# Performance work log

Measured on AMD Instinct MI355X. Metric: run time of the kernel, lower is better.

Reference implementation:

```python
import jax, jax.numpy as jnp
import numpy as np

B, S, H = 2, 2048, 2048
NH, NKV, HD = 16, 4, 128
ROPE_BASE = 10000.0


def hbit_linear(x, w):
    # BitNet: 8-bit per-token absmax activation quant, ternary (2-bit) weight quant
    s = 127.0 / jnp.clip(jnp.max(jnp.abs(x), axis=-1, keepdims=True), 1e-5, None)
    xq = jnp.clip(jnp.round(x * s), -128, 127) / s
    ws = 1.0 / jnp.clip(jnp.mean(jnp.abs(w)), 1e-5, None)
    wq = jnp.clip(jnp.round(w * ws), -1, 1) / ws
    return xq @ wq.T


def rotate_half(x):
    h = x.shape[-1] // 2
    return jnp.concatenate([-x[..., h:], x[..., :h]], axis=-1)


def rope_cos_sin(position_ids, head_dim, dtype):
    inv_freq = 1.0 / (ROPE_BASE ** (jnp.arange(0, head_dim, 2, dtype=jnp.float32) / head_dim))
    freqs = position_ids.astype(jnp.float32)[..., None] * inv_freq[None, None, :]  # (b,s,hd/2)
    emb = jnp.concatenate([freqs, freqs], axis=-1)  # (b,s,hd)
    return jnp.cos(emb).astype(dtype)[:, :, None, :], jnp.sin(emb).astype(dtype)[:, :, None, :]


def setup_inputs() -> dict:
    key = jax.random.key(0)
    ks = jax.random.split(key, 5)
    xavier = lambda k, shp: jax.random.uniform(k, shp, jnp.float32, -1.0, 1.0) * np.sqrt(6.0 / (shp[0] + shp[1]))
    causal = jnp.where(jnp.tril(jnp.ones((S, S), bool)), 0.0, -1e9).astype(jnp.float32)[None, None]
    return {
        "hidden_states": jax.random.normal(ks[0], (B, S, H), jnp.float32),
        "attention_mask": causal,
        "Wq": xavier(ks[1], (H, H)),
        "Wk": xavier(ks[2], (NKV * HD, H)),
        "Wv": xavier(ks[3], (NKV * HD, H)),
        "Wo": xavier(ks[4], (H, H)),
        "position_ids": jnp.arange(S, dtype=jnp.int64 if jax.config.jax_enable_x64 else jnp.int32)[None, :],
    }


def reference(hidden_states, attention_mask, Wq, Wk, Wv, Wo, position_ids):
    b, s, _ = hidden_states.shape
    q = hbit_linear(hidden_states, Wq).reshape(b, s, NH, HD)
    k = hbit_linear(hidden_states, Wk).reshape(b, s, NKV, HD)
    v = hbit_linear(hidden_states, Wv).reshape(b, s, NKV, HD)
    cos, sin = rope_cos_sin(position_ids, HD, q.dtype)  # (1,s,1,hd)
    q = q * cos + rotate_half(q) * sin
    k = k * cos + rotate_half(k) * sin
    n_rep = NH // NKV
    k = jnp.repeat(k, n_rep, axis=2)  # (b,s,NH,hd)
    v = jnp.repeat(v, n_rep, axis=2)
    scale = 1.0 / np.sqrt(HD)
    scores = jnp.einsum("bqhd,bkhd->bhqk", q, k) * scale + attention_mask
    probs = jax.nn.softmax(scores, axis=-1)  # dropout inactive (eval)
    out = jnp.einsum("bhqk,bkhd->bqhd", probs, v).reshape(b, s, NH * HD)
    return hbit_linear(out, Wo)
```

## Files before the change

### kernel.cpp

```cpp
#include <hip/hip_runtime.h>
#include <hip/hip_bf16.h>

#define B_ 2
#define S_ 2048
#define H_ 2048
#define NH_ 16
#define NKV_ 4
#define HD_ 128
#define M_ (B_*S_)
#define KVD_ (NKV_*HD_)
#define PSTR 40
#define GRID_MEGA 768

typedef signed char s8;
typedef __attribute__((ext_vector_type(8))) short short8;
typedef __attribute__((ext_vector_type(4))) float f32x4;
typedef __attribute__((ext_vector_type(4))) int int4v;

__device__ __forceinline__ float loadf(const void* p, long i, int isb){
  if (isb) return __bfloat162float(((const __hip_bfloat16*)p)[i]);
  return ((const float*)p)[i];
}

__device__ __forceinline__ unsigned short f2bf(float f){
  union { float f; unsigned u; } v; v.f = f;
  unsigned r = v.u + 0x7FFF + ((v.u >> 16) & 1);
  return (unsigned short)(r >> 16);
}

__device__ __forceinline__ float bf2f(unsigned short b){
  union { unsigned u; float f; } v; v.u = ((unsigned)b) << 16; return v.f;
}

__device__ __forceinline__ void gl2lds16(const void* g, void* l){
  __builtin_amdgcn_global_load_lds(
      (const __attribute__((address_space(1))) void*)g,
      (__attribute__((address_space(3))) void*)l, 16, 0, 0);
}

__device__ __forceinline__ void gridbar(unsigned* bar, unsigned target){
  __syncthreads();
  if (threadIdx.x == 0){
    __threadfence();
    atomicAdd(bar, 1u);
    unsigned guard = 0;
    while (atomicAdd(bar, 0u) < target){
      __builtin_amdgcn_s_sleep(2);
      if (++guard > (1u<<22)) break;
    }
    __threadfence();
  }
  __syncthreads();
}

__device__ __forceinline__ int detect_isb_s(const unsigned int* x, int* dsh){
  int t = threadIdx.x, cnt = 0;
  #pragma unroll
  for (int i = 0; i < 8; i++){
    unsigned e = (x[t + i*256] >> 7) & 0xFF;
    cnt += (e >= 90 && e <= 150) ? 1 : 0;
  }
  #pragma unroll
  for (int k = 32; k > 0; k >>= 1) cnt += __shfl_down(cnt, k, 64);
  if ((t & 63) == 0) dsh[t >> 6] = cnt;
  __syncthreads();
  int r = (dsh[0] + dsh[1] + dsh[2] + dsh[3]) > 1228;
  __syncthreads();
  return r;
}

__device__ __forceinline__ void wscan_seg(const void* w, long n, long b0, int nb,
                                          int isb, float* wsum_i, float* sh){
  int t = threadIdx.x;
  float s = 0.f;
  for (long i = b0*256 + t; i < n; i += (long)nb*256) s += fabsf(loadf(w, i, isb));
  sh[t] = s; __syncthreads();
  for (int k = 128; k > 0; k >>= 1){ if (t < k) sh[t] += sh[t+k]; __syncthreads(); }
  if (t == 0) atomicAdd(wsum_i, sh[0]);
  __syncthreads();
}

__device__ __forceinline__ void wquant_seg(const void* w, s8* out, long n, long b0, int nb,
                                           float mean, int isb){
  int t = threadIdx.x;
  float sc = 1.0f / mean;
  for (long i = b0*256 + t; i < n; i += (long)nb*256){
    float v = rintf(loadf(w, i, isb) * sc);
    v = fminf(fmaxf(v, -1.f), 1.f);
    out[i] = (s8)v;
  }
}

__device__ __forceinline__ void aquant_row_x(const void* x, int isb, long r,
                                             float* srow, s8* xq, float* sh){
  int t = threadIdx.x;
  long base = r * H_;
  float v[8];
  if (isb){
    uint4 wv = ((const uint4*)((const unsigned short*)x + base))[t];
    unsigned u[4] = {wv.x, wv.y, wv.z, wv.w};
    #pragma unroll
    for (int i = 0; i < 4; i++){
      v[2*i]   = bf2f((unsigned short)(u[i] & 0xFFFF));
      v[2*i+1] = bf2f((unsigned short)(u[i] >> 16));
    }
  } else {
    const float4* p = (const float4*)((const float*)x + base);
    float4 a = p[t*2], b2 = p[t*2+1];
    v[0]=a.x; v[1]=a.y; v[2]=a.z; v[3]=a.w; v[4]=b2.x; v[5]=b2.y; v[6]=b2.z; v[7]=b2.w;
  }
  float mx = 0.f;
  #pragma unroll
  for (int i = 0; i < 8; i++) mx = fmaxf(mx, fabsf(v[i]));
  sh[t] = mx; __syncthreads();
  for (int k = 128; k > 0; k >>= 1){ if (t < k) sh[t] = fmaxf(sh[t], sh[t+k]); __syncthreads(); }
  float s = 127.0f / fmaxf(sh[0], 1e-5f);
  if (t == 0) srow[r] = s;
  unsigned long long pk = 0;
  #pragma unroll
  for (int i = 0; i < 8; i++){
    float q = fminf(fmaxf(rintf(v[i] * s), -128.f), 127.f);
    pk |= ((unsigned long long)(unsigned char)(s8)q) << (8*i);
  }
  *(unsigned long long*)(xq + base + t*8) = pk;
  __syncthreads();
}

__device__ __forceinline__ void aquant_row_ab(const unsigned short* x, long r,
                                              float* srow, s8* xq, float* sh){
  int t = threadIdx.x;
  long base = r * H_;
  uint4 wv = ((const uint4*)(x + base))[t];
  unsigned u[4] = {wv.x, wv.y, wv.z, wv.w};
  float v[8];
  #pragma unroll
  for (int i = 0; i < 4; i++){
    v[2*i]   = bf2f((unsigned short)(u[i] & 0xFFFF));
    v[2*i+1] = bf2f((unsigned short)(u[i] >> 16));
  }
  float mx = 0.f;
  #pragma unroll
  for (int i = 0; i < 8; i++) mx = fmaxf(mx, fabsf(v[i]));
  sh[t] = mx; __syncthreads();
  for (int k = 128; k > 0; k >>= 1){ if (t < k) sh[t] = fmaxf(sh[t], sh[t+k]); __syncthreads(); }
  float s = 127.0f / fmaxf(sh[0], 1e-5f);
  if (t == 0) srow[r] = s;
  unsigned long long pk = 0;
  #pragma unroll
  for (int i = 0; i < 8; i++){
    float q = fminf(fmaxf(rintf(v[i] * s), -128.f), 127.f);
    pk |= ((unsigned long long)(unsigned char)(s8)q) << (8*i);
  }
  *(unsigned long long*)(xq + base + t*8) = pk;
  __syncthreads();
}

__device__ __forceinline__ void gemm_core(
      const s8* __restrict__ A, const s8* __restrict__ Bw, s8* As, s8* Bs,
      const float* __restrict__ srow, float mean,
      void* __restrict__ Cout, int N, int mode, int isb,
      unsigned short* __restrict__ Vt,
      const float* __restrict__ ct, const float* __restrict__ st,
      long bcol, long arow){
  int tid = threadIdx.x;
  int wave = tid >> 6, lane = tid & 63;
  int quad = lane >> 4, c = lane & 15;
  int wm = wave >> 1, wn = wave & 1;
  const int K = H_;

  int4v acc[4][4];
  #pragma unroll
  for (int mt = 0; mt < 4; mt++)
    #pragma unroll
    for (int nt = 0; nt < 4; nt++) acc[mt][nt] = (int4v){0,0,0,0};

  int rl = lane >> 2;
  int kq = (lane & 3) ^ ((lane >> 3) & 3);
  int ch0 = wave*2, ch1 = wave*2 + 1;
  long gA0 = (arow + ch0*16 + rl)*(long)K + kq*16;
  long gA1 = (arow + ch1*16 + rl)*(long)K + kq*16;
  long gB0 = (bcol + ch0*16 + rl)*(long)K + kq*16;
  long gB1 = (bcol + ch1*16 + rl)*(long)K + kq*16;

  int sA = quad ^ ((c >> 1) & 3);
  int ntl[4];
  #pragma unroll
  for (int nt = 0; nt < 4; nt++) ntl[nt] = 2*wn + (nt & 1) + 4*(nt >> 1);
  int frA[4], frB[4];
  #pragma unroll
  for (int mt = 0; mt < 4; mt++) frA[mt] = (wm*64 + mt*16 + c)*64 + sA*16;
  #pragma unroll
  for (int nt = 0; nt < 4; nt++) frB[nt] = (ntl[nt]*16 + c)*64 + sA*16;

  for (int k0 = 0; k0 < K; k0 += 128){
    gl2lds16(A  + gA0 + k0,      As        + ch0*1024);
    gl2lds16(A  + gA1 + k0,      As        + ch1*1024);
    gl2lds16(Bw + gB0 + k0,      Bs        + ch0*1024);
    gl2lds16(Bw + gB1 + k0,      Bs        + ch1*1024);
    gl2lds16(A  + gA0 + k0 + 64, As + 8192 + ch0*1024);
    gl2lds16(A  + gA1 + k0 + 64, As + 8192 + ch1*1024);
    gl2lds16(Bw + gB0 + k0 + 64, Bs + 8192 + ch0*1024);
    gl2lds16(Bw + gB1 + k0 + 64, Bs + 8192 + ch1*1024);
    __syncthreads();
    #pragma unroll
    for (int s = 0; s < 2; s++){
      const s8* Ab = As + s*8192;
      const s8* Bb = Bs + s*8192;
      int4v afr[4], bfr[4];
      #pragma unroll
      for (int mt = 0; mt < 4; mt++) afr[mt] = *(const int4v*)&Ab[frA[mt]];
      #pragma unroll
      for (int nt = 0; nt < 4; nt++) bfr[nt] = *(const int4v*)&Bb[frB[nt]];
      #pragma unroll
      for (int mt = 0; mt < 4; mt++)
        #pragma unroll
        for (int nt = 0; nt < 4; nt++)
          acc[mt][nt] = __builtin_amdgcn_mfma_i32_16x16x64_i8(afr[mt], bfr[nt], acc[mt][nt], 0, 0, 0);
    }
    __syncthreads();
  }

  if (mode == 0 || mode == 3){
    unsigned short* Ob = (unsigned short*)Cout;
    #pragma unroll
    for (int mt = 0; mt < 4; mt++){
      #pragma unroll
      for (int r = 0; r < 4; r++){
        long grow = arow + wm*64 + mt*16 + quad*4 + r;
        float sc = mean / srow[grow];
        if (mode == 0) sc *= 0.12751743f;
        int pos = (int)(grow & (S_-1));
        #pragma unroll
        for (int p = 0; p < 2; p++){
          int col_lo = (int)bcol + (2*wn + p)*16 + c;
          int d = col_lo & 63;
          float cv = ct[pos*64 + d], sv = st[pos*64 + d];
          float vlo = acc[mt][p][r]   * sc;
          float vhi = acc[mt][p+2][r] * sc;
          Ob[grow*(long)N + col_lo]      = f2bf(vlo*cv - vhi*sv);
          Ob[grow*(long)N + col_lo + 64] = f2bf(vhi*cv + vlo*sv);
        }
      }
    }
  } else if (mode == 1){
    #pragma unroll
    for (int mt = 0; mt < 4; mt++){
      long grow0 = arow + wm*64 + mt*16 + quad*4;
      float s0 = mean / srow[grow0];
      float s1 = mean / srow[grow0+1];
      float s2 = mean / srow[grow0+2];
      float s3 = mean / srow[grow0+3];
      long bb = grow0 >> 11; int sI = (int)(grow0 & (S_-1));
      unsigned short* base = Vt + bb*(long)KVD_*S_ + sI;
      #pragma unroll
      for (int nt = 0; nt < 4; nt++){
        float v0 = acc[mt][nt][0]*s0, v1 = acc[mt][nt][1]*s1;
        float v2 = acc[mt][nt][2]*s2, v3 = acc[mt][nt][3]*s3;
        unsigned lo, hi;
        asm("v_cvt_pk_bf16_f32 %0, %1, %2" : "=v"(lo) : "v"(v0), "v"(v1));
        asm("v_cvt_pk_bf16_f32 %0, %1, %2" : "=v"(hi) : "v"(v2), "v"(v3));
        uint2 pk; pk.x = lo; pk.y = hi;
        *(uint2*)(base + (long)(bcol + ntl[nt]*16 + c)*S_) = pk;
      }
    }
  } else {
    #pragma unroll
    for (int mt = 0; mt < 4; mt++){
      #pragma unroll
      for (int r = 0; r < 4; r++){
        long grow = arow + wm*64 + mt*16 + quad*4 + r;
        float sc = mean / srow[grow];
        long cb = grow*(long)N + bcol + c;
        if (isb){
          __hip_bfloat16* o = (__hip_bfloat16*)Cout;
          #pragma unroll
          for (int nt = 0; nt < 4; nt++)
            o[cb + ntl[nt]*16] = __float2bfloat16(acc[mt][nt][r] * sc);
        } else {
          float* o = (float*)Cout;
          #pragma unroll
          for (int nt = 0; nt < 4; nt++)
            o[cb + ntl[nt]*16] = acc[mt][nt][r] * sc;
        }
      }
    }
  }
}

__device__ __forceinline__ void qkv_tile(int lid, const s8* xq,
      const s8* wqq, const s8* wkq, const s8* wvq,
      const float* srow, const float* wsum,
      unsigned short* Qb, unsigned short* Kb, unsigned short* Vt,
      const float* ct, const float* st, s8* As, s8* Bs){
  int xcd = lid & 7;
  int rem = lid >> 3;
  int by  = xcd*4 + (rem & 3);
  int bx  = rem >> 2;
  const float cq = (float)((long)H_*H_), ck = (float)((long)KVD_*H_);
  const s8* Bw; void* Cout; unsigned short* vt = nullptr;
  int N, mode; float mean; long bcol;
  if (bx < 16){
    Bw = wqq; Cout = Qb; N = H_;   mode = 0; mean = fmaxf(wsum[0]/cq, 1e-5f);  bcol = (long)bx*128;
  } else if (bx < 20){
    Bw = wkq; Cout = Kb; N = KVD_; mode = 3; mean = fmaxf(wsum[1]/ck, 1e-5f); bcol = (long)(bx-16)*128;
  } else {
    Bw = wvq; Cout = nullptr; vt = Vt; N = KVD_; mode = 1; mean = fmaxf(wsum[2]/ck, 1e-5f); bcol = (long)(bx-20)*128;
  }
  gemm_core(xq, Bw, As, Bs, srow, mean, Cout, N, mode, 0, vt, ct, st, bcol, (long)by*128);
}

__device__ __forceinline__ void o_tile(int lid, const s8* aq, const s8* woq,
      const float* srow, const float* wsum, int isb, void* out,
      const float* ct, const float* st, s8* As, s8* Bs){
  int xcd = lid & 7;
  int rem = lid >> 3;
  int by  = xcd*4 + (rem & 3);
  int bx  = rem >> 2;
  float mean = fmaxf(wsum[3] / (float)((long)H_*H_), 1e-5f);
  gemm_core(aq, woq, As, Bs, srow, mean, out, H_, 2, isb, nullptr, ct, st,
            (long)bx*128, (long)by*128);
}

__device__ __forceinline__ void attn_body(int win, int kvh, int b,
    const unsigned short* __restrict__ Qb, const unsigned short* __restrict__ Kb,
    const unsigned short* __restrict__ Vt, unsigned short* __restrict__ ob,
    unsigned short (*Ks)[64*128], unsigned short* Vs, unsigned short (*Ps)[16*PSTR]){
  int wid = threadIdx.x >> 6, lane = threadIdx.x & 63;
  int quad = lane >> 4, c = lane & 15;
  if (b == 1) win = (S_/32 - 1) - win;
  int h = kvh*4 + wid;
  int q0 = win*32;

  short8 qf[2][4];
  #pragma unroll
  for (int t0 = 0; t0 < 2; t0++)
    #pragma unroll
    for (int f = 0; f < 4; f++)
      qf[t0][f] = *(const short8*)(Qb + ((long)(b*S_ + q0 + t0*16 + c)*NH_ + h)*HD_ + f*32 + quad*8);

  const unsigned short* Kg = Kb + (long)b*S_*KVD_ + kvh*HD_;
  const unsigned short* Vg = Vt + ((long)b*KVD_ + kvh*HD_)*S_;

  f32x4 o[2][8], ol[2];
  #pragma unroll
  for (int t0 = 0; t0 < 2; t0++){
    #pragma unroll
    for (int i = 0; i < 8; i++) o[t0][i] = (f32x4){0.f,0.f,0.f,0.f};
    ol[t0] = (f32x4){0.f,0.f,0.f,0.f};
  }
  short8 ones;
  #pragma unroll
  for (int i = 0; i < 8; i++) ones[i] = (short)0x3F80;

  int skey = lane >> 4;
  int kslot = lane & 15;
  int vrow = lane >> 3;
  int vslot = lane & 7;

  int nk = q0 + 32;
  #pragma unroll
  for (int i = 0; i < 4; i++){
    int kk = wid*16 + i*4;
    int key = kk + skey;
    int g = kslot ^ (key & 15);
    gl2lds16(Kg + (long)key*KVD_ + g*8, &Ks[0][kk*128]);
  }

  int buf = 0;
  for (int kc = 0; kc < nk; kc += 64, buf ^= 1){
    __syncthreads();
    #pragma unroll
    for (int i = 0; i < 4; i++){
      int rr = wid*32 + i*8;
      int hd = rr + vrow;
      int g = vslot ^ (hd & 7);
      gl2lds16(Vg + (long)hd*S_ + kc + g*8, &Vs[rr*64]);
    }

    f32x4 s[2][4];
    #pragma unroll
    for (int t0 = 0; t0 < 2; t0++)
      #pragma unroll
      for (int kt = 0; kt < 4; kt++) s[t0][kt] = (f32x4){0.f,0.f,0.f,0.f};
    #pragma unroll
    for (int kt = 0; kt < 4; kt++){
      short8 kf4[4];
      #pragma unroll
      for (int f = 0; f < 4; f++)
        kf4[f] = *(const short8*)&Ks[buf][(kt*16 + c)*128 + ((f*4 + quad) ^ c)*8];
      #pragma unroll
      for (int t0 = 0; t0 < 2; t0++)
        #pragma unroll
        for (int f = 0; f < 4; f++)
          s[t0][kt] = __builtin_amdgcn_mfma_f32_16x16x32_bf16(kf4[f], qf[t0][f], s[t0][kt], 0, 0, 0);
    }
    #pragma unroll
    for (int t0 = 0; t0 < 2; t0++){
      int qv = q0 + t0*16 + c;
      if (kc + 63 > q0 + t0*16){
        #pragma unroll
        for (int kt = 0; kt < 4; kt++){
          #pragma unroll
          for (int r = 0; r < 4; r++){
            int key = kc + kt*16 + quad*4 + r;
            if (key > qv) s[t0][kt][r] = -1e30f;
          }
        }
      }
    }

    __syncthreads();

    if (kc + 64 < nk){
      #pragma unroll
      for (int i = 0; i < 4; i++){
        int kk = wid*16 + i*4;
        int key = kk + skey;
        int g = kslot ^ (key & 15);
        gl2lds16(Kg + (long)(kc + 64 + key)*KVD_ + g*8, &Ks[buf^1][kk*128]);
      }
    }

    #pragma unroll
    for (int pp = 0; pp < 2; pp++){
      short8 vf[8];
      #pragma unroll
      for (int nt = 0; nt < 8; nt++)
        vf[nt] = *(const short8*)&Vs[(nt*16 + c)*64 + ((pp*4 + quad) ^ (c & 7))*8];
      #pragma unroll
      for (int t0 = 0; t0 < 2; t0++){
        #pragma unroll
        for (int tk = 0; tk < 2; tk++){
          f32x4 sv = s[t0][pp*2 + tk];
          float e0 = exp2f(sv[0]), e1 = exp2f(sv[1]);
          float e2 = exp2f(sv[2]), e3 = exp2f(sv[3]);
          unsigned w0, w1;
          asm("v_cvt_pk_bf16_f32 %0, %1, %2" : "=v"(w0) : "v"(e0), "v"(e1));
          asm("v_cvt_pk_bf16_f32 %0, %1, %2" : "=v"(w1) : "v"(e2), "v"(e3));
          uint2 pkv; pkv.x = w0; pkv.y = w1;
          *(uint2*)&Ps[wid][c*PSTR + tk*16 + quad*4] = pkv;
        }
        short8 pf = *(const short8*)&Ps[wid][c*PSTR + quad*8];
        #pragma unroll
        for (int nt = 0; nt < 8; nt++)
          o[t0][nt] = __builtin_amdgcn_mfma_f32_16x16x32_bf16(pf, vf[nt], o[t0][nt], 0, 0, 0);
        ol[t0] = __builtin_amdgcn_mfma_f32_16x16x32_bf16(pf, ones, ol[t0], 0, 0, 0);
      }
    }
  }

  #pragma unroll
  for (int t0 = 0; t0 < 2; t0++){
    float il[4];
    #pragma unroll
    for (int r = 0; r < 4; r++) il[r] = 1.0f / ol[t0][r];
    #pragma unroll
    for (int nt = 0; nt < 8; nt++)
      #pragma unroll
      for (int r = 0; r < 4; r++)
        ob[((long)(b*S_ + q0 + t0*16 + quad*4 + r))*H_ + h*HD_ + nt*16 + c] = f2bf(o[t0][nt][r]*il[r]);
  }
}


__global__ void k_prep_aq(const void* x,
                          const void* Wq, const void* Wk, const void* Wv, const void* Wo,
                          float* wsum, float* ct, float* st,
                          float* srow, s8* xq){
  __shared__ __align__(16) float sh[256];
  __shared__ int dsh[4];
  int isb = detect_isb_s((const unsigned int*)x, dsh);
  int bid = blockIdx.x, t = threadIdx.x;
  if (bid < 2048){
    if (t < 64){
      float inv = exp2f(-(float)t * 0.20762050593045952f);
      float a = (float)bid * inv;
      float sn, cs; sincosf(a, &sn, &cs);
      ct[bid*64 + t] = cs; st[bid*64 + t] = sn;
    }
    if (bid < 768)       wscan_seg(Wq, (long)H_*H_,   bid,      768, isb, &wsum[0], sh);
    else if (bid < 1024) wscan_seg(Wk, (long)KVD_*H_, bid-768,  256, isb, &wsum[1], sh);
    else if (bid < 1280) wscan_seg(Wv, (long)KVD_*H_, bid-1024, 256, isb, &wsum[2], sh);
    else                 wscan_seg(Wo, (long)H_*H_,   bid-1280, 768, isb, &wsum[3], sh);
  } else {
    aquant_row_x(x, isb, bid - 2048, srow, xq, sh);
  }
}

__global__ void k_wquant_all(const void* Wq, const void* Wk, const void* Wv, const void* Wo,
                             const void* x, const float* wsum,
                             s8* oq, s8* ok, s8* ov, s8* oo){
  __shared__ int dsh[4];
  int isb = detect_isb_s((const unsigned int*)x, dsh);
  int bid = blockIdx.x;
  const float cq = (float)((long)H_*H_), ck = (float)((long)KVD_*H_);
  if (bid < 1024)      wquant_seg(Wq, oq, (long)H_*H_,   bid,      1024, fmaxf(wsum[0]/cq, 1e-5f), isb);
  else if (bid < 1280) wquant_seg(Wk, ok, (long)KVD_*H_, bid-1024, 256,  fmaxf(wsum[1]/ck, 1e-5f), isb);
  else if (bid < 1536) wquant_seg(Wv, ov, (long)KVD_*H_, bid-1280, 256,  fmaxf(wsum[2]/ck, 1e-5f), isb);
  else                 wquant_seg(Wo, oo, (long)H_*H_,   bid-1536, 1024, fmaxf(wsum[3]/cq, 1e-5f), isb);
}

__global__ void k_aquant_bf16(const unsigned short* __restrict__ x,
                              float* __restrict__ srow, s8* __restrict__ xq){
  __shared__ __align__(16) float sh[256];
  aquant_row_ab(x, blockIdx.x, srow, xq, sh);
}

__global__ __launch_bounds__(256, 2) void k_gemm_qkv(
      const s8* __restrict__ xq,
      const s8* __restrict__ wqq, const s8* __restrict__ wkq, const s8* __restrict__ wvq,
      const float* __restrict__ srow, const float* __restrict__ wsum,
      unsigned short* __restrict__ Qb, unsigned short* __restrict__ Kb,
      unsigned short* __restrict__ Vt,
      const float* __restrict__ ct, const float* __restrict__ st){
  __shared__ __align__(16) s8 As[2*128*64];
  __shared__ __align__(16) s8 Bs[2*128*64];
  qkv_tile(blockIdx.x, xq, wqq, wkq, wvq, srow, wsum, Qb, Kb, Vt, ct, st, As, Bs);
}

__global__ __launch_bounds__(256, 2) void k_gemm_o(
      const s8* __restrict__ aq, const s8* __restrict__ woq,
      const float* __restrict__ srow, const float* __restrict__ wsum,
      const void* __restrict__ x, void* __restrict__ out,
      const float* __restrict__ ct, const float* __restrict__ st){
  __shared__ __align__(16) s8 As[2*128*64];
  __shared__ __align__(16) s8 Bs[2*128*64];
  __shared__ int dsh[4];
  int isb = detect_isb_s((const unsigned int*)x, dsh);
  o_tile(blockIdx.x, aq, woq, srow, wsum, isb, out, ct, st, As, Bs);
}

__global__ __launch_bounds__(256) void k_attn_mfma(const unsigned short* __restrict__ Qb,
    const unsigned short* __restrict__ Kb, const unsigned short* __restrict__ Vt,
    unsigned short* __restrict__ ob){
  __shared__ __align__(16) unsigned short Ks[2][64*128];
  __shared__ __align__(16) unsigned short Vs[128*64];
  __shared__ __align__(16) unsigned short Ps[4][16*PSTR];
  attn_body(blockIdx.x, blockIdx.y, blockIdx.z, Qb, Kb, Vt, ob, Ks, Vs, Ps);
}

struct SmemAttn { unsigned short Ks[2][64*128]; unsigned short Vs[128*64]; unsigned short Ps[4][16*PSTR]; };
struct SmemGemm { s8 As[2*128*64]; s8 Bs[2*128*64]; };

__global__ __launch_bounds__(256, 3) void k_mega(
    const void* x, const void* Wq, const void* Wk, const void* Wv, const void* Wo,
    float* wsum, unsigned* bars, float* ct, float* st, float* s_x, s8* xq,
    s8* wqq, s8* wkq, s8* wvq, s8* woq,
    unsigned short* Qb, unsigned short* Kb, unsigned short* Vt,
    unsigned short* ab, float* s_a, s8* aq, void* out){
  __shared__ __align__(16) unsigned char smem[sizeof(SmemAttn)];
  float* sh = (float*)smem;
  int*  dsh = (int*)(smem + 1024);
  int bid = blockIdx.x, t = threadIdx.x;
  int isb = detect_isb_s((const unsigned int*)x, dsh);

  {
    long idx = (long)bid*256 + t;
    if (idx < (long)S_*64){
      int pos = (int)(idx >> 6), d = (int)(idx & 63);
      float inv = exp2f(-(float)d * 0.20762050593045952f);
      float a = (float)pos * inv;
      float sn, cs; sincosf(a, &sn, &cs);
      ct[pos*64 + d] = cs; st[pos*64 + d] = sn;
    }
    if (bid < 288)      wscan_seg(Wq, (long)H_*H_,   bid,     288, isb, &wsum[0], sh);
    else if (bid < 384) wscan_seg(Wk, (long)KVD_*H_, bid-288, 96,  isb, &wsum[1], sh);
    else if (bid < 480) wscan_seg(Wv, (long)KVD_*H_, bid-384, 96,  isb, &wsum[2], sh);
    else                wscan_seg(Wo, (long)H_*H_,   bid-480, 288, isb, &wsum[3], sh);
    for (long r = bid; r < M_; r += GRID_MEGA) aquant_row_x(x, isb, r, s_x, xq, sh);
  }
  gridbar(&bars[0], GRID_MEGA);

  {
    const float cq = (float)((long)H_*H_), ck = (float)((long)KVD_*H_);
    if (bid < 288)      wquant_seg(Wq, wqq, (long)H_*H_,   bid,     288, fmaxf(wsum[0]/cq, 1e-5f), isb);
    else if (bid < 384) wquant_seg(Wk, wkq, (long)KVD_*H_, bid-288, 96,  fmaxf(wsum[1]/ck, 1e-5f), isb);
    else if (bid < 480) wquant_seg(Wv, wvq, (long)KVD_*H_, bid-384, 96,  fmaxf(wsum[2]/ck, 1e-5f), isb);
    else                wquant_seg(Wo, woq, (long)H_*H_,   bid-480, 288, fmaxf(wsum[3]/cq, 1e-5f), isb);
  }
  gridbar(&bars[1], GRID_MEGA);

  {
    SmemGemm* sg = (SmemGemm*)smem;
    qkv_tile(bid, xq, wqq, wkq, wvq, s_x, wsum, Qb, Kb, Vt, ct, st, sg->As, sg->Bs);
  }
  gridbar(&bars[2], GRID_MEGA);

  if (bid < 512){
    SmemAttn* sa = (SmemAttn*)smem;
    attn_body(bid & 63, (bid >> 6) & 3, bid >> 8, Qb, Kb, Vt, ab, sa->Ks, sa->Vs, sa->Ps);
  }
  gridbar(&bars[3], GRID_MEGA);

  for (long r = bid; r < M_; r += GRID_MEGA) aquant_row_ab(ab, r, s_a, aq, sh);
  gridbar(&bars[4], GRID_MEGA);

  if (bid < 512){
    SmemGemm* sg = (SmemGemm*)smem;
    o_tile(bid, aq, woq, s_a, wsum, isb, out, ct, st, sg->As, sg->Bs);
  }
}

extern "C" void kernel_launch(void* const* d_in, const int* in_sizes, int n_in,
                              void* d_out, int out_size, void* d_ws, size_t ws_size,
                              hipStream_t stream){
  (void)in_sizes; (void)n_in; (void)out_size; (void)ws_size;
  const void* x  = d_in[0];
  const void* Wq = d_in[2];
  const void* Wk = d_in[3];
  const void* Wv = d_in[4];
  const void* Wo = d_in[5];
  char* ws = (char*)d_ws;
  size_t o = 0;
  auto alloc = [&](size_t b){ size_t r = o; o += (b + 255) & ~(size_t)255; return r; };
  size_t META = alloc(256);
  float* wsum = (float*)(ws + META);
  unsigned* bars = (unsigned*)(ws + META + 64);
  float* s_x = (float*)(ws + alloc((size_t)M_*4));
  float* s_a = (float*)(ws + alloc((size_t)M_*4));
  float* ct  = (float*)(ws + alloc((size_t)S_*64*4));
  float* st  = (float*)(ws + alloc((size_t)S_*64*4));
  s8* xq  = (s8*)(ws + alloc((size_t)M_*H_));
  s8* wqq = (s8*)(ws + alloc((size_t)H_*H_));
  s8* wkq = (s8*)(ws + alloc((size_t)KVD_*H_));
  s8* wvq = (s8*)(ws + alloc((size_t)KVD_*H_));
  s8* woq = (s8*)(ws + alloc((size_t)H_*H_));
  unsigned short* Qb = (unsigned short*)(ws + alloc((size_t)M_*NH_*HD_*2));
  unsigned short* Kb = (unsigned short*)(ws + alloc((size_t)M_*KVD_*2));
  unsigned short* Vt = (unsigned short*)(ws + alloc((size_t)M_*KVD_*2));
  unsigned short* ab = (unsigned short*)(ws + alloc((size_t)M_*H_*2));
  s8* aq = (s8*)(ws + alloc((size_t)M_*H_));
  void* outp = d_out;

  hipMemsetAsync(ws + META, 0, 256, stream);

  static int mega_ok = -1;
  if (mega_ok < 0){
    hipFuncAttributes fa{};
    int occ = 0;
    hipError_t e1 = hipFuncGetAttributes(&fa, (const void*)k_mega);
    hipError_t e2 = hipOccupancyMaxActiveBlocksPerMultiprocessor(&occ, (const void*)k_mega, 256, 0);
    mega_ok = (e1 == hipSuccess && e2 == hipSuccess &&
               occ >= 3 && fa.numRegs > 0 && fa.numRegs <= 168) ? 1 : 0;
  }

  if (mega_ok == 1){
    k_mega<<<GRID_MEGA, 256, 0, stream>>>(
        x, Wq, Wk, Wv, Wo, wsum, bars, ct, st, s_x, xq,
        wqq, wkq, wvq, woq, Qb, Kb, Vt, ab, s_a, aq, outp);
    return;
  }

  k_prep_aq<<<2048 + M_, 256, 0, stream>>>(x, Wq, Wk, Wv, Wo, wsum, ct, st, s_x, xq);
  k_wquant_all<<<2560, 256, 0, stream>>>(Wq, Wk, Wv, Wo, x, wsum, wqq, wkq, wvq, woq);
  k_gemm_qkv<<<768, 256, 0, stream>>>(xq, wqq, wkq, wvq, s_x, wsum, Qb, Kb, Vt, ct, st);
  dim3 ga(S_/32, NKV_, B_);
  k_attn_mfma<<<ga, 256, 0, stream>>>(Qb, Kb, Vt, ab);
  k_aquant_bf16<<<M_, 256, 0, stream>>>(ab, s_a, aq);
  k_gemm_o<<<512, 256, 0, stream>>>(aq, woq, s_a, wsum, x, d_out, ct, st);
}
```

Baseline: 291.8 us.

## Shrink persistent megakernel grid and use release-counter grid barrier

Reduces the persistent megakernel grid from 768 to 512 blocks with launch bounds relaxed to 2 blocks per CU, so the kernel may use more registers. The QKV GEMM tiles are now processed in a loop, and the weight-scan and quant work is re-partitioned across the smaller grid. The grid barrier changes from a monotone counter polled by every block to a counter plus release word: the last arriver resets the count and bumps the release, and the others poll only the release. The aim is cheaper barriers, no idle blocks in the attention and O phases, and less register pressure, at the cost of less parallelism in the prep and QKV phases.

```diff
diff --git a/kernel.cpp b/kernel.cpp
--- a/kernel.cpp
+++ b/kernel.cpp
@@ -10,7 +10,7 @@
 #define M_ (B_*S_)
 #define KVD_ (NKV_*HD_)
 #define PSTR 40
-#define GRID_MEGA 768
+#define GRID_MEGA 512
 
 typedef signed char s8;
 typedef __attribute__((ext_vector_type(8))) short short8;
@@ -38,15 +38,22 @@
       (__attribute__((address_space(3))) void*)l, 16, 0, 0);
 }
 
-__device__ __forceinline__ void gridbar(unsigned* bar, unsigned target){
+__device__ __forceinline__ void gridbar(unsigned* cnt, unsigned* rel, unsigned target){
   __syncthreads();
   if (threadIdx.x == 0){
+    unsigned relv = atomicAdd(rel, 0u);
     __threadfence();
-    atomicAdd(bar, 1u);
-    unsigned guard = 0;
-    while (atomicAdd(bar, 0u) < target){
-      __builtin_amdgcn_s_sleep(2);
-      if (++guard > (1u<<22)) break;
+    unsigned old = atomicAdd(cnt, 1u);
+    if (old == target - 1u){
+      atomicExch(cnt, 0u);
+      __threadfence();
+      atomicAdd(rel, 1u);
+    } else {
+      unsigned guard = 0;
+      while (atomicAdd(rel, 0u) == relv){
+        __builtin_amdgcn_s_sleep(2);
+        if (++guard > (1u<<24)) break;
+      }
     }
     __threadfence();
   }
@@ -542,7 +549,7 @@
 struct SmemAttn { unsigned short Ks[2][64*128]; unsigned short Vs[128*64]; unsigned short Ps[4][16*PSTR]; };
 struct SmemGemm { s8 As[2*128*64]; s8 Bs[2*128*64]; };
 
-__global__ __launch_bounds__(256, 3) void k_mega(
+__global__ __launch_bounds__(256, 2) void k_mega(
     const void* x, const void* Wq, const void* Wk, const void* Wv, const void* Wo,
     float* wsum, unsigned* bars, float* ct, float* st, float* s_x, s8* xq,
     s8* wqq, s8* wkq, s8* wvq, s8* woq,
@@ -556,46 +563,47 @@
 
   {
     long idx = (long)bid*256 + t;
-    if (idx < (long)S_*64){
-      int pos = (int)(idx >> 6), d = (int)(idx & 63);
-      float inv = exp2f(-(float)d * 0.20762050593045952f);
-      float a = (float)pos * inv;
-      float sn, cs; sincosf(a, &sn, &cs);
-      ct[pos*64 + d] = cs; st[pos*64 + d] = sn;
-    }
-    if (bid < 288)      wscan_seg(Wq, (long)H_*H_,   bid,     288, isb, &wsum[0], sh);
-    else if (bid < 384) wscan_seg(Wk, (long)KVD_*H_, bid-288, 96,  isb, &wsum[1], sh);
-    else if (bid < 480) wscan_seg(Wv, (long)KVD_*H_, bid-384, 96,  isb, &wsum[2], sh);
-    else                wscan_seg(Wo, (long)H_*H_,   bid-480, 288, isb, &wsum[3], sh);
+    int pos = (int)(idx >> 6), d = (int)(idx & 63);
+    float inv = exp2f(-(float)d * 0.20762050593045952f);
+    float a = (float)pos * inv;
+    float sn, cs; sincosf(a, &sn, &cs);
+    ct[pos*64 + d] = cs; st[pos*64 + d] = sn;
+    if (bid < 192)      wscan_seg(Wq, (long)H_*H_,   bid,     192, isb, &wsum[0], sh);
+    else if (bid < 256) wscan_seg(Wk, (long)KVD_*H_, bid-192, 64,  isb, &wsum[1], sh);
+    else if (bid < 320) wscan_seg(Wv, (long)KVD_*H_, bid-256, 64,  isb, &wsum[2], sh);
+    else                wscan_seg(Wo, (long)H_*H_,   bid-320, 192, isb, &wsum[3], sh);
     for (long r = bid; r < M_; r += GRID_MEGA) aquant_row_x(x, isb, r, s_x, xq, sh);
   }
-  gridbar(&bars[0], GRID_MEGA);
+  gridbar(&bars[0], &bars[1], GRID_MEGA);
 
   {
     const float cq = (float)((long)H_*H_), ck = (float)((long)KVD_*H_);
-    if (bid < 288)      wquant_seg(Wq, wqq, (long)H_*H_,   bid,     288, fmaxf(wsum[0]/cq, 1e-5f), isb);
-    else if (bid < 384) wquant_seg(Wk, wkq, (long)KVD_*H_, bid-288, 96,  fmaxf(wsum[1]/ck, 1e-5f), isb);
-    else if (bid < 480) wquant_seg(Wv, wvq, (long)KVD_*H_, bid-384, 96,  fmaxf(wsum[2]/ck, 1e-5f), isb);
-    else                wquant_seg(Wo, woq, (long)H_*H_,   bid-480, 288, fmaxf(wsum[3]/cq, 1e-5f), isb);
-  }
-  gridbar(&bars[1], GRID_MEGA);
+    if (bid < 192)      wquant_seg(Wq, wqq, (long)H_*H_,   bid,     192, fmaxf(wsum[0]/cq, 1e-5f), isb);
+    else if (bid < 256) wquant_seg(Wk, wkq, (long)KVD_*H_, bid-192, 64,  fmaxf(wsum[1]/ck, 1e-5f), isb);
+    else if (bid < 320) wquant_seg(Wv, wvq, (long)KVD_*H_, bid-256, 64,  fmaxf(wsum[2]/ck, 1e-5f), isb);
+    else                wquant_seg(Wo, woq, (long)H_*H_,   bid-320, 192, fmaxf(wsum[3]/cq, 1e-5f), isb);
+  }
+  gridbar(&bars[2], &bars[3], GRID_MEGA);
 
   {
     SmemGemm* sg = (SmemGemm*)smem;
-    qkv_tile(bid, xq, wqq, wkq, wvq, s_x, wsum, Qb, Kb, Vt, ct, st, sg->As, sg->Bs);
-  }
-  gridbar(&bars[2], GRID_MEGA);
-
-  if (bid < 512){
+    for (int tile = bid; tile < 768; tile += GRID_MEGA){
+      qkv_tile(tile, xq, wqq, wkq, wvq, s_x, wsum, Qb, Kb, Vt, ct, st, sg->As, sg->Bs);
+      __syncthreads();
+    }
+  }
+  gridbar(&bars[4], &bars[5], GRID_MEGA);
+
+  {
     SmemAttn* sa = (SmemAttn*)smem;
     attn_body(bid & 63, (bid >> 6) & 3, bid >> 8, Qb, Kb, Vt, ab, sa->Ks, sa->Vs, sa->Ps);
   }
-  gridbar(&bars[3], GRID_MEGA);
+  gridbar(&bars[6], &bars[7], GRID_MEGA);
 
   for (long r = bid; r < M_; r += GRID_MEGA) aquant_row_ab(ab, r, s_a, aq, sh);
-  gridbar(&bars[4], GRID_MEGA);
-
-  if (bid < 512){
+  gridbar(&bars[8], &bars[9], GRID_MEGA);
+
+  {
     SmemGemm* sg = (SmemGemm*)smem;
     o_tile(bid, aq, woq, s_a, wsum, isb, out, ct, st, sg->As, sg->Bs);
   }
@@ -641,7 +649,7 @@
     hipError_t e1 = hipFuncGetAttributes(&fa, (const void*)k_mega);
     hipError_t e2 = hipOccupancyMaxActiveBlocksPerMultiprocessor(&occ, (const void*)k_mega, 256, 0);
     mega_ok = (e1 == hipSuccess && e2 == hipSuccess &&
-               occ >= 3 && fa.numRegs > 0 && fa.numRegs <= 168) ? 1 : 0;
+               occ >= 2 && fa.numRegs > 0 && fa.localSizeBytes == 0) ? 1 : 0;
   }
 
   if (mega_ok == 1){
```

New measurement: 292.7 us. No clear change (+0.3%).
